# Kernel optimization log

Hardware: AMD Instinct MI355X
Metric: run time of the kernel (lower is better)

Reference implementation:

```python
import jax, jax.numpy as jnp
import numpy as np

B, D, N, E = 4, 8, 2000, 32000
EMB, H, C = 32, 4, 32  # in_channels == embedding_dim == out_channels per head
NEG_SLOPE = 0.2        # PyG GATConv default


def setup_inputs() -> dict:
    key = jax.random.key(0)
    ks = jax.random.split(key, 7)
    x = jax.random.randint(ks[0], (B, D, N), 0, N)              # congestion tokens
    adjacency = jax.random.randint(ks[1], (2, E), 0, N)         # shared edge_index
    emb_table = jax.random.normal(ks[2], (N, EMB), jnp.float32)
    lin_w = jax.random.normal(ks[3], (EMB, H * C), jnp.float32) / np.sqrt(EMB)
    att_src = jax.random.normal(ks[4], (H, C), jnp.float32) / np.sqrt(C)
    att_dst = jax.random.normal(ks[5], (H, C), jnp.float32) / np.sqrt(C)
    bias = jnp.zeros((H * C,), jnp.float32)
    return {"x": x, "adjacency": adjacency, "emb_table": emb_table,
            "lin_w": lin_w, "att_src": att_src, "att_dst": att_dst, "bias": bias}


def reference(x, adjacency, emb_table, lin_w, att_src, att_dst, bias):
    Bb, Dd, Nn = x.shape
    G = Bb * Dd
    # embedding lookup -> [G, N, EMB]
    h = emb_table[x].reshape(G, Nn, EMB)
    # GATConv linear transform -> [G, N, H, C]
    hl = jnp.einsum('gnd,dhc->gnhc', h, lin_w.reshape(EMB, H, C))
    # add self loops (PyG add_self_loops=True)
    loops = jnp.arange(Nn)
    src = jnp.concatenate([adjacency[0], loops])
    dst = jnp.concatenate([adjacency[1], loops])
    # per-node attention logits [G, N, H]
    a_src = jnp.einsum('gnhc,hc->gnh', hl, att_src)
    a_dst = jnp.einsum('gnhc,hc->gnh', hl, att_dst)

    def one_graph(xh, asrc, adst):
        # edge-wise logits (messages flow src -> dst)
        e = jax.nn.leaky_relu(asrc[src] + adst[dst], NEG_SLOPE)          # [Et, H]
        m = jax.ops.segment_max(e, dst, num_segments=Nn)                 # [N, H]
        ex = jnp.exp(e - m[dst])
        s = jax.ops.segment_sum(ex, dst, num_segments=Nn)                # [N, H]
        alpha = ex / s[dst]                                              # segment softmax
        msg = alpha[:, :, None] * xh[src]                                # [Et, H, C]
        return jax.ops.segment_sum(msg, dst, num_segments=Nn)            # [N, H, C]

    out = jax.vmap(one_graph)(hl, a_src, a_dst)                          # [G, N, H, C]
    out = out.reshape(G, Nn, H * C) + bias                               # concat heads + bias
    return out.reshape(Bb, Dd, Nn * H * C)
```

## Files before the change

### kernel.cpp

```cpp
#include <hip/hip_runtime.h>
#include <hip/hip_bf16.h>

#define NODES  2000
#define GRAPHS 32
#define NEDGE  32000
#define EMBD   32
#define HEADS  4
#define CDIM   32
#define HC     128
#define DCAP   64
#define NEG_SLOPE 0.2f

__device__ unsigned short g_tb[NODES * HC];
__device__ float g_ts[NODES * HEADS];
__device__ float g_td[NODES * HEADS];
__device__ int   g_cnt[NODES];
__device__ int   g_slot[NODES * DCAP];

__device__ __forceinline__ float lrelu(float z) {
    return z >= 0.f ? z : NEG_SLOPE * z;
}
__device__ __forceinline__ float bflo(unsigned int w) {
    return __uint_as_float(w << 16);
}
__device__ __forceinline__ float bfhi(unsigned int w) {
    return __uint_as_float(w & 0xffff0000u);
}

__global__ __launch_bounds__(256) void k_prep(
    const float* __restrict__ emb,
    const float* __restrict__ lw,
    const float* __restrict__ asrc,
    const float* __restrict__ adst,
    const int*   __restrict__ adj)
{
    if (blockIdx.x >= NODES / 2) {
        int e = (blockIdx.x - NODES / 2) * 256 + threadIdx.x;
        int s = adj[e];
        int d = adj[NEDGE + e];
        int pos = atomicAdd(&g_cnt[d], 1);
        if (pos < DCAP) g_slot[d * DCAP + pos] = s;
        return;
    }

    int v = blockIdx.x * 2 + (threadIdx.x >> 7);
    int j = threadIdx.x & 127;

    float acc = 0.f;
#pragma unroll
    for (int d = 0; d < EMBD; ++d)
        acc = fmaf(emb[v * EMBD + d], lw[d * HC + j], acc);
    g_tb[v * HC + j] = (unsigned short)(__bfloat16_as_ushort(__float2bfloat16(acc)));

    int h = j >> 5, c = j & 31;
    float ps = acc * asrc[h * CDIM + c];
    float pd = acc * adst[h * CDIM + c];
#pragma unroll
    for (int m = 16; m >= 1; m >>= 1) {
        ps += __shfl_xor(ps, m);
        pd += __shfl_xor(pd, m);
    }
    if (c == 0) {
        g_ts[v * HEADS + h] = ps;
        g_td[v * HEADS + h] = pd;
    }
}

__global__ __launch_bounds__(256) void k_main(
    const int* __restrict__ x,
    const float* __restrict__ bias,
    float* __restrict__ out)
{
    int gid = blockIdx.x * 16 + (threadIdx.x >> 4);
    int t   = threadIdx.x & 15;
    int g = gid / NODES;
    int n = gid - g * NODES;
    int h  = t >> 2;
    int j0 = t * 8;

    const int* xg = x + g * NODES;
    int tokn = xg[n];
    float ad = g_td[tokn * HEADS + h];

    int deg = g_cnt[n];
    if (deg > DCAP) deg = DCAP;
    const int* sl = g_slot + n * DCAP;

    float wself = __expf(lrelu(g_ts[tokn * HEADS + h] + ad));
    float ssum = wself;
    float a0, a1, a2, a3, a4, a5, a6, a7;
    {
        uint4 r = *(const uint4*)(g_tb + tokn * HC + j0);
        a0 = wself * bflo(r.x); a1 = wself * bfhi(r.x);
        a2 = wself * bflo(r.y); a3 = wself * bfhi(r.y);
        a4 = wself * bflo(r.z); a5 = wself * bfhi(r.z);
        a6 = wself * bflo(r.w); a7 = wself * bfhi(r.w);
    }

    if (deg > 0) {
        int last = deg - 1;
        int sB   = sl[min(1, last)];
        int tkA  = xg[sl[0]];
        float tsA = g_ts[tkA * HEADS + h];
        uint4 rA  = *(const uint4*)(g_tb + tkA * HC + j0);
        int tkB  = xg[sB];
        for (int p = 0; p <= last; ++p) {
            int sC = sl[min(p + 2, last)];
            float tsB = g_ts[tkB * HEADS + h];
            uint4 rB  = *(const uint4*)(g_tb + tkB * HC + j0);
            int tkC = xg[sC];

            float w = __expf(lrelu(tsA + ad));
            ssum += w;
            a0 = fmaf(w, bflo(rA.x), a0); a1 = fmaf(w, bfhi(rA.x), a1);
            a2 = fmaf(w, bflo(rA.y), a2); a3 = fmaf(w, bfhi(rA.y), a3);
            a4 = fmaf(w, bflo(rA.z), a4); a5 = fmaf(w, bfhi(rA.z), a5);
            a6 = fmaf(w, bflo(rA.w), a6); a7 = fmaf(w, bfhi(rA.w), a7);

            tkA = tkB; tsA = tsB; rA = rB; tkB = tkC;
        }
    }

    float inv = 1.f / ssum;
    const float4* bp = (const float4*)(bias + j0);
    float4 b0 = bp[0], b1 = bp[1];
    float4 o0, o1;
    o0.x = fmaf(a0, inv, b0.x); o0.y = fmaf(a1, inv, b0.y);
    o0.z = fmaf(a2, inv, b0.z); o0.w = fmaf(a3, inv, b0.w);
    o1.x = fmaf(a4, inv, b1.x); o1.y = fmaf(a5, inv, b1.y);
    o1.z = fmaf(a6, inv, b1.z); o1.w = fmaf(a7, inv, b1.w);

    float4* op = (float4*)(out + (size_t)gid * HC + j0);
    op[0] = o0;
    op[1] = o1;
}

__global__ void k_reset()
{
    int i = blockIdx.x * 256 + threadIdx.x;
    if (i < NODES) g_cnt[i] = 0;
}

extern "C" void kernel_launch(void* const* d_in, const int* in_sizes, int n_in,
                              void* d_out, int out_size, void* d_ws, size_t ws_size,
                              hipStream_t stream)
{
    (void)in_sizes; (void)n_in; (void)out_size; (void)d_ws; (void)ws_size;

    const int*   x    = (const int*)d_in[0];
    const int*   adj  = (const int*)d_in[1];
    const float* emb  = (const float*)d_in[2];
    const float* lw   = (const float*)d_in[3];
    const float* asrc = (const float*)d_in[4];
    const float* adst = (const float*)d_in[5];
    const float* bias = (const float*)d_in[6];
    float*       out  = (float*)d_out;

    k_prep <<<NODES / 2 + NEDGE / 256, 256, 0, stream>>>(emb, lw, asrc, adst, adj);
    k_main <<<(GRAPHS * NODES) / 16, 256, 0, stream>>>(x, bias, out);
    k_reset<<<(NODES + 255) / 256, 256, 0, stream>>>();
}
```

Before: 118.0 us.

## Interleave graphs per node in work mapping and unroll edge loop by two

Work items are remapped so consecutive groups handle the same destination node across the 32 graphs instead of consecutive nodes of one graph. Neighbors of a block then share slot lists and degree, which should improve cache reuse and reduce divergence in loop trip counts. The edge loop now processes two edges per iteration with deeper prefetch to raise memory-level parallelism. Output writes become strided across graphs, which costs some write coalescing between groups.

```diff
diff --git a/kernel.cpp b/kernel.cpp
--- a/kernel.cpp
+++ b/kernel.cpp
@@ -50,7 +50,7 @@
 #pragma unroll
     for (int d = 0; d < EMBD; ++d)
         acc = fmaf(emb[v * EMBD + d], lw[d * HC + j], acc);
-    g_tb[v * HC + j] = (unsigned short)(__bfloat16_as_ushort(__float2bfloat16(acc)));
+    g_tb[v * HC + j] = __bfloat16_as_ushort(__float2bfloat16(acc));
 
     int h = j >> 5, c = j & 31;
     float ps = acc * asrc[h * CDIM + c];
@@ -71,10 +71,10 @@
     const float* __restrict__ bias,
     float* __restrict__ out)
 {
-    int gid = blockIdx.x * 16 + (threadIdx.x >> 4);
-    int t   = threadIdx.x & 15;
-    int g = gid / NODES;
-    int n = gid - g * NODES;
+    int i = blockIdx.x * 16 + (threadIdx.x >> 4);
+    int t = threadIdx.x & 15;
+    int n = i >> 5;
+    int g = i & 31;
     int h  = t >> 2;
     int j0 = t * 8;
 
@@ -99,25 +99,37 @@
 
     if (deg > 0) {
         int last = deg - 1;
-        int sB   = sl[min(1, last)];
-        int tkA  = xg[sl[0]];
-        float tsA = g_ts[tkA * HEADS + h];
-        uint4 rA  = *(const uint4*)(g_tb + tkA * HC + j0);
-        int tkB  = xg[sB];
-        for (int p = 0; p <= last; ++p) {
-            int sC = sl[min(p + 2, last)];
-            float tsB = g_ts[tkB * HEADS + h];
-            uint4 rB  = *(const uint4*)(g_tb + tkB * HC + j0);
-            int tkC = xg[sC];
+        int t0 = xg[sl[0]];
+        int t1 = xg[sl[min(1, last)]];
+        uint4 r0 = *(const uint4*)(g_tb + t0 * HC + j0);
+        uint4 r1 = *(const uint4*)(g_tb + t1 * HC + j0);
+        float s0 = g_ts[t0 * HEADS + h];
+        float s1 = g_ts[t1 * HEADS + h];
+        int t2 = xg[sl[min(2, last)]];
+        int t3 = xg[sl[min(3, last)]];
+        for (int p = 0; p <= last; p += 2) {
+            uint4 r2 = *(const uint4*)(g_tb + t2 * HC + j0);
+            uint4 r3 = *(const uint4*)(g_tb + t3 * HC + j0);
+            float s2 = g_ts[t2 * HEADS + h];
+            float s3 = g_ts[t3 * HEADS + h];
+            int t4 = xg[sl[min(p + 4, last)]];
+            int t5 = xg[sl[min(p + 5, last)]];
 
-            float w = __expf(lrelu(tsA + ad));
-            ssum += w;
-            a0 = fmaf(w, bflo(rA.x), a0); a1 = fmaf(w, bfhi(rA.x), a1);
-            a2 = fmaf(w, bflo(rA.y), a2); a3 = fmaf(w, bfhi(rA.y), a3);
-            a4 = fmaf(w, bflo(rA.z), a4); a5 = fmaf(w, bfhi(rA.z), a5);
-            a6 = fmaf(w, bflo(rA.w), a6); a7 = fmaf(w, bfhi(rA.w), a7);
+            float w0 = __expf(lrelu(s0 + ad));
+            float w1 = __expf(lrelu(s1 + ad));
+            w1 = (p + 1 <= last) ? w1 : 0.f;
+            ssum += w0 + w1;
+            a0 = fmaf(w0, bflo(r0.x), fmaf(w1, bflo(r1.x), a0));
+            a1 = fmaf(w0, bfhi(r0.x), fmaf(w1, bfhi(r1.x), a1));
+            a2 = fmaf(w0, bflo(r0.y), fmaf(w1, bflo(r1.y), a2));
+            a3 = fmaf(w0, bfhi(r0.y), fmaf(w1, bfhi(r1.y), a3));
+            a4 = fmaf(w0, bflo(r0.z), fmaf(w1, bflo(r1.z), a4));
+            a5 = fmaf(w0, bfhi(r0.z), fmaf(w1, bfhi(r1.z), a5));
+            a6 = fmaf(w0, bflo(r0.w), fmaf(w1, bflo(r1.w), a6));
+            a7 = fmaf(w0, bfhi(r0.w), fmaf(w1, bfhi(r1.w), a7));
 
-            tkA = tkB; tsA = tsB; rA = rB; tkB = tkC;
+            t0 = t2; t1 = t3; r0 = r2; r1 = r3; s0 = s2; s1 = s3;
+            t2 = t4; t3 = t5;
         }
     }
 
@@ -130,7 +142,7 @@
     o1.x = fmaf(a4, inv, b1.x); o1.y = fmaf(a5, inv, b1.y);
     o1.z = fmaf(a6, inv, b1.z); o1.w = fmaf(a7, inv, b1.w);
 
-    float4* op = (float4*)(out + (size_t)gid * HC + j0);
+    float4* op = (float4*)(out + ((size_t)g * NODES + n) * HC + j0);
     op[0] = o0;
     op[1] = o1;
 }
```

After: 111.0 us. 1.06x faster.

## Remap main kernel to one node across 16 graphs and precompute edge weights in LDS

Applied to the files above, without the earlier changes.

Each block now handles a single destination node for 16 graphs. It first cooperatively computes all edge attention weights (all four heads) and source tokens into shared memory, then each 16-thread group aggregates messages using a deeper 4-stage prefetch of feature rows. This shares the slot list and per-edge exp work across graphs and removes the dependent x/g_ts loads from the inner loop. The cost is a block-wide barrier, LDS usage, and output writes that are no longer contiguous per block.

```diff
diff --git a/kernel.cpp b/kernel.cpp
--- a/kernel.cpp
+++ b/kernel.cpp
@@ -50,7 +50,7 @@
 #pragma unroll
     for (int d = 0; d < EMBD; ++d)
         acc = fmaf(emb[v * EMBD + d], lw[d * HC + j], acc);
-    g_tb[v * HC + j] = (unsigned short)(__bfloat16_as_ushort(__float2bfloat16(acc)));
+    g_tb[v * HC + j] = __bfloat16_as_ushort(__float2bfloat16(acc));
 
     int h = j >> 5, c = j & 31;
     float ps = acc * asrc[h * CDIM + c];
@@ -71,20 +71,43 @@
     const float* __restrict__ bias,
     float* __restrict__ out)
 {
-    int gid = blockIdx.x * 16 + (threadIdx.x >> 4);
-    int t   = threadIdx.x & 15;
-    int g = gid / NODES;
-    int n = gid - g * NODES;
-    int h  = t >> 2;
-    int j0 = t * 8;
+    __shared__ float l_w[DCAP * 16 * 4];
+    __shared__ int   l_tok[DCAP * 16];
 
-    const int* xg = x + g * NODES;
-    int tokn = xg[n];
-    float ad = g_td[tokn * HEADS + h];
+    int b = blockIdx.x;
+    int n = b >> 1;
+    int gset = (b & 1) << 4;
 
     int deg = g_cnt[n];
     if (deg > DCAP) deg = DCAP;
     const int* sl = g_slot + n * DCAP;
+
+    for (int i = threadIdx.x; i < deg * 16; i += 256) {
+        int p = i >> 4, g = i & 15;
+        const int* xg = x + (gset + g) * NODES;
+        int s   = sl[p];
+        int tok = xg[s];
+        int tkn = xg[n];
+        float4 ts4 = *(const float4*)(g_ts + tok * HEADS);
+        float4 td4 = *(const float4*)(g_td + tkn * HEADS);
+        float4 w4;
+        w4.x = __expf(lrelu(ts4.x + td4.x));
+        w4.y = __expf(lrelu(ts4.y + td4.y));
+        w4.z = __expf(lrelu(ts4.z + td4.z));
+        w4.w = __expf(lrelu(ts4.w + td4.w));
+        *(float4*)(l_w + (size_t)i * 4) = w4;
+        l_tok[i] = tok;
+    }
+    __syncthreads();
+
+    int gl = threadIdx.x >> 4;
+    int t  = threadIdx.x & 15;
+    int h  = t >> 2;
+    int j0 = t * 8;
+
+    const int* xg = x + (gset + gl) * NODES;
+    int tokn = xg[n];
+    float ad = g_td[tokn * HEADS + h];
 
     float wself = __expf(lrelu(g_ts[tokn * HEADS + h] + ad));
     float ssum = wself;
@@ -99,25 +122,33 @@
 
     if (deg > 0) {
         int last = deg - 1;
-        int sB   = sl[min(1, last)];
-        int tkA  = xg[sl[0]];
-        float tsA = g_ts[tkA * HEADS + h];
-        uint4 rA  = *(const uint4*)(g_tb + tkA * HC + j0);
-        int tkB  = xg[sB];
+        int q0 = l_tok[0 * 16 + gl];
+        int q1 = l_tok[min(1, last) * 16 + gl];
+        int q2 = l_tok[min(2, last) * 16 + gl];
+        int q3 = l_tok[min(3, last) * 16 + gl];
+        uint4 R0 = *(const uint4*)(g_tb + q0 * HC + j0);
+        uint4 R1 = *(const uint4*)(g_tb + q1 * HC + j0);
+        uint4 R2 = *(const uint4*)(g_tb + q2 * HC + j0);
+        uint4 R3 = *(const uint4*)(g_tb + q3 * HC + j0);
+        int q4 = l_tok[min(4, last) * 16 + gl];
+        int q5 = l_tok[min(5, last) * 16 + gl];
+        float wA = l_w[(0 * 16 + gl) * 4 + h];
+        float wB = l_w[(min(1, last) * 16 + gl) * 4 + h];
+
         for (int p = 0; p <= last; ++p) {
-            int sC = sl[min(p + 2, last)];
-            float tsB = g_ts[tkB * HEADS + h];
-            uint4 rB  = *(const uint4*)(g_tb + tkB * HC + j0);
-            int tkC = xg[sC];
+            uint4 Rn = *(const uint4*)(g_tb + q4 * HC + j0);
+            int   qn = l_tok[min(p + 6, last) * 16 + gl];
+            float wn = l_w[(min(p + 2, last) * 16 + gl) * 4 + h];
 
-            float w = __expf(lrelu(tsA + ad));
-            ssum += w;
-            a0 = fmaf(w, bflo(rA.x), a0); a1 = fmaf(w, bfhi(rA.x), a1);
-            a2 = fmaf(w, bflo(rA.y), a2); a3 = fmaf(w, bfhi(rA.y), a3);
-            a4 = fmaf(w, bflo(rA.z), a4); a5 = fmaf(w, bfhi(rA.z), a5);
-            a6 = fmaf(w, bflo(rA.w), a6); a7 = fmaf(w, bfhi(rA.w), a7);
+            ssum += wA;
+            a0 = fmaf(wA, bflo(R0.x), a0); a1 = fmaf(wA, bfhi(R0.x), a1);
+            a2 = fmaf(wA, bflo(R0.y), a2); a3 = fmaf(wA, bfhi(R0.y), a3);
+            a4 = fmaf(wA, bflo(R0.z), a4); a5 = fmaf(wA, bfhi(R0.z), a5);
+            a6 = fmaf(wA, bflo(R0.w), a6); a7 = fmaf(wA, bfhi(R0.w), a7);
 
-            tkA = tkB; tsA = tsB; rA = rB; tkB = tkC;
+            R0 = R1; R1 = R2; R2 = R3; R3 = Rn;
+            q4 = q5; q5 = qn;
+            wA = wB; wB = wn;
         }
     }
 
@@ -130,7 +161,7 @@
     o1.x = fmaf(a4, inv, b1.x); o1.y = fmaf(a5, inv, b1.y);
     o1.z = fmaf(a6, inv, b1.z); o1.w = fmaf(a7, inv, b1.w);
 
-    float4* op = (float4*)(out + (size_t)gid * HC + j0);
+    float4* op = (float4*)(out + ((size_t)(gset + gl) * NODES + n) * HC + j0);
     op[0] = o0;
     op[1] = o1;
 }
@@ -157,6 +188,6 @@
     float*       out  = (float*)d_out;
 
     k_prep <<<NODES / 2 + NEDGE / 256, 256, 0, stream>>>(emb, lw, asrc, adst, adj);
-    k_main <<<(GRAPHS * NODES) / 16, 256, 0, stream>>>(x, bias, out);
+    k_main <<<GRAPHS * NODES / 16, 256, 0, stream>>>(x, bias, out);
     k_reset<<<(NODES + 255) / 256, 256, 0, stream>>>();
 }
```

Result: faster. 109.6 us (-7.1%).
